# Kernel tuning notes

Measured on AMD Instinct MI355X. Metric: run time of the kernel, lower is better.

The kernel has to match this reference:

```python
import jax, jax.numpy as jnp
import numpy as np

# Pitch / YIN hyperparameters (match init_kwargs)
SR = 8000
HOP = int(round(0.01 * SR))        # 80 samples per hop (hop_time=0.01)
F0_MIN = 60
F0_MAX = 400
THRESH = 0.2
TAU_MIN = SR // F0_MAX             # 20  (smallest lag / highest pitch)
TAU_MAX = SR // F0_MIN             # 133 (largest lag / lowest pitch)
W = TAU_MAX                        # YIN integration window
FRAME_LEN = 2 * TAU_MAX            # need W + TAU_MAX samples per frame


def _yin_f0(x):
    """Batched YIN pitch estimator. x: [B, n_samples] -> f0: [B, n_frames-1].

    Vectorizes the original per-sample Python loop over the whole batch and
    all frames in one pass (difference fn -> CMNDF -> thresholded lag pick).
    """
    B, n = x.shape
    n_frames = 1 + (n - FRAME_LEN) // HOP

    # Frame the signal: [B, F, FRAME_LEN]
    starts = jnp.arange(n_frames) * HOP
    idx = starts[:, None] + jnp.arange(FRAME_LEN)[None, :]
    frames = x[:, idx]

    # Difference function d(tau) = sum_j (x[j] - x[j+tau])^2, tau in [0, TAU_MAX]
    taus = jnp.arange(TAU_MAX + 1)
    sidx = taus[:, None] + jnp.arange(W)[None, :]          # [T+1, W]
    shifted = frames[:, :, sidx]                           # [B, F, T+1, W]
    base = frames[:, :, None, :W]                          # [B, F, 1,  W]
    d = jnp.sum((base - shifted) ** 2, axis=-1)            # [B, F, T+1]

    # Cumulative-mean-normalized difference function (CMNDF)
    eps = jnp.asarray(1e-8, x.dtype)
    cum = jnp.cumsum(d[..., 1:], axis=-1)
    tnum = jnp.arange(1, TAU_MAX + 1, dtype=x.dtype)
    cmndf = d[..., 1:] * tnum / jnp.maximum(cum, eps)      # tau = 1..TAU_MAX
    cmndf = jnp.concatenate([jnp.ones_like(cmndf[..., :1]), cmndf], axis=-1)

    # First lag below threshold (restricted to valid pitch range); else unvoiced
    tau_idx = jnp.arange(TAU_MAX + 1)
    cand = (cmndf < THRESH) & (tau_idx >= TAU_MIN)         # [B, F, T+1]
    voiced = jnp.any(cand, axis=-1)
    tau = jnp.argmax(cand, axis=-1)                        # first True
    f0 = jnp.where(
        voiced,
        jnp.asarray(SR, x.dtype) / jnp.maximum(tau, 1).astype(x.dtype),
        jnp.zeros((), x.dtype),
    )
    # Original forward drops the last frame per sample: f0[0, :-1]
    return f0[:, :-1]


def setup_inputs() -> dict:
    key = jax.random.key(0)
    x = jax.random.normal(key, (8, 80000), dtype=jnp.float32)
    return {"x": x}


def reference(x):
    return _yin_f0(x)
```

## Files before the change

### kernel.cpp

```cpp
#include <hip/hip_runtime.h>


#define NF_OUT 996
#define NSAMP  80000
#define FPB    6
#define BPB    (NF_OUT / FPB)
#define CHUNKD 672
#define TH     0.2f
#define EPS    1e-8f

template<int CTRL>
__device__ __forceinline__ float dpp_add_f(float x) {
    int t = __builtin_amdgcn_update_dpp(0, __builtin_bit_cast(int, x), CTRL, 0xF, 0xF, false);
    return x + __builtin_bit_cast(float, t);
}
__device__ __forceinline__ float dpp_b15_add_f(float x) {
    int t = __builtin_amdgcn_update_dpp(0, __builtin_bit_cast(int, x), 0x142, 0xA, 0xF, false);
    return x + __builtin_bit_cast(float, t);
}
template<int CTRL>
__device__ __forceinline__ int dpp_min_i(int x) {
    int t = __builtin_amdgcn_update_dpp(0x7FFFFFFF, x, CTRL, 0xF, 0xF, false);
    return (t < x) ? t : x;
}
__device__ __forceinline__ int dpp_b15_min_i(int x) {
    int t = __builtin_amdgcn_update_dpp(0x7FFFFFFF, x, 0x142, 0xA, 0xF, false);
    return (t < x) ? t : x;
}
__device__ __forceinline__ float scan32_add(float v) {
    v = dpp_add_f<0x111>(v);
    v = dpp_add_f<0x112>(v);
    v = dpp_add_f<0x114>(v);
    v = dpp_add_f<0x118>(v);
    v = dpp_b15_add_f(v);
    return v;
}
__device__ __forceinline__ int red32_min(int v) {
    v = dpp_min_i<0x111>(v);
    v = dpp_min_i<0x112>(v);
    v = dpp_min_i<0x114>(v);
    v = dpp_min_i<0x118>(v);
    v = dpp_b15_min_i(v);
    return v;
}

#define MAC4(CURV, NXTV, FRV) do {                                             \
    float w0=CURV.y,w1=CURV.z,w2=CURV.w,w3=NXTV.x,w4=NXTV.y,w5=NXTV.z,w6=NXTV.w; \
    float d_;                                                                  \
    d_=FRV.x-w0; a0=fmaf(d_,d_,a0); d_=FRV.y-w1; a0=fmaf(d_,d_,a0);            \
    d_=FRV.z-w2; a0=fmaf(d_,d_,a0); d_=FRV.w-w3; a0=fmaf(d_,d_,a0);            \
    d_=FRV.x-w1; a1=fmaf(d_,d_,a1); d_=FRV.y-w2; a1=fmaf(d_,d_,a1);            \
    d_=FRV.z-w3; a1=fmaf(d_,d_,a1); d_=FRV.w-w4; a1=fmaf(d_,d_,a1);            \
    d_=FRV.x-w2; a2=fmaf(d_,d_,a2); d_=FRV.y-w3; a2=fmaf(d_,d_,a2);            \
    d_=FRV.z-w4; a2=fmaf(d_,d_,a2); d_=FRV.w-w5; a2=fmaf(d_,d_,a2);            \
    d_=FRV.x-w3; a3=fmaf(d_,d_,a3); d_=FRV.y-w4; a3=fmaf(d_,d_,a3);            \
    d_=FRV.z-w5; a3=fmaf(d_,d_,a3); d_=FRV.w-w6; a3=fmaf(d_,d_,a3);            \
} while (0)

__global__ __launch_bounds__(192) void yin_kernel(const float* __restrict__ x,
                                                  float* __restrict__ out) {
    const int bx = blockIdx.x;
    const int b  = bx / BPB;
    const int fb = bx - b * BPB;
    const float* __restrict__ xrow = x + (size_t)b * NSAMP + (size_t)fb * (FPB * 80);

    __shared__ __align__(16) float sch[CHUNKD];
    const int t = threadIdx.x;
    {
        int t4 = t * 4;
        if (t4 < CHUNKD)
            *(float4*)(sch + t4) = *(const float4*)(xrow + t4);
    }
    __syncthreads();

    const int lane = t & 63;
    const int w    = t >> 6;
    const int h    = lane >> 5;
    const int l2   = lane & 31;
    const float* f  = sch + (2 * w + h) * 80;
    const float* gp = f + 4 * l2;

    float4 cur = *(const float4*)(gp);
    const float4 S0 = cur;
    float4 nxt;
    float a0 = 0.f, a1 = 0.f, a2 = 0.f, a3 = 0.f;

    #pragma unroll 4
    for (int c = 0; c < 32; ++c) {
        nxt = *(const float4*)(gp + 4 * (c + 1));
        float4 fr = *(const float4*)(f + 4 * c);
        MAC4(cur, nxt, fr);
        cur = nxt;
    }
    const float4 C32 = cur;
    {
        nxt = *(const float4*)(gp + 4 * 33);
        float4 fr = *(const float4*)(f + 128);
        MAC4(cur, nxt, fr);
        cur = nxt;
    }
    const float4 C33 = cur;
    const float4 C34 = *(const float4*)(gp + 4 * 34);
    {
        float frx = f[132];
        float d_;
        d_ = frx - C33.y; a0 = fmaf(d_, d_, a0);
        d_ = frx - C33.z; a1 = fmaf(d_, d_, a1);
        d_ = frx - C33.w; a2 = fmaf(d_, d_, a2);
        d_ = frx - C34.x; a3 = fmaf(d_, d_, a3);
    }

    float sm[8] = {C32.y, C32.z, C32.w, C33.x, C33.y, C33.z, C33.w, C34.x};
    float s0a[4] = {S0.x, S0.y, S0.z, S0.w};
    float p[5] = {0.f, 0.f, 0.f, 0.f, 0.f};
    #pragma unroll
    for (int k = 0; k < 5; ++k) {
        #pragma unroll
        for (int q = 0; q < 4; ++q) {
            float d_ = s0a[q] - sm[k + q];
            p[k] = fmaf(d_, d_, p[k]);
        }
    }
    if (l2 < 5) {
        float av = f[128 + l2];
        #pragma unroll
        for (int k = 0; k < 5; ++k) {
            float d_ = av - f[257 + l2 + k];
            p[k] = fmaf(d_, d_, p[k]);
        }
    }
    #pragma unroll
    for (int k = 0; k < 5; ++k) p[k] = scan32_add(p[k]);

    float L = a0 + a1 + a2 + a3;
    float inc = scan32_add(L);
    float excl = inc - L;
    float c0 = excl + a0;
    float c1 = c0 + a1;
    float c2 = c1 + a2;
    float c3 = c2 + a3;

    int best = 0x7FFFFFFF;
    const int tau0 = 4 * l2 + 1;
    if (tau0     >= 20 && a0 * (float)(tau0)     < TH * fmaxf(c0, EPS)) best = tau0;
    if (best == 0x7FFFFFFF && tau0 + 1 >= 20 && a1 * (float)(tau0 + 1) < TH * fmaxf(c1, EPS)) best = tau0 + 1;
    if (best == 0x7FFFFFFF && tau0 + 2 >= 20 && a2 * (float)(tau0 + 2) < TH * fmaxf(c2, EPS)) best = tau0 + 2;
    if (best == 0x7FFFFFFF && tau0 + 3 >= 20 && a3 * (float)(tau0 + 3) < TH * fmaxf(c3, EPS)) best = tau0 + 3;

    if (l2 == 31) {
        float cum = c3;
        #pragma unroll
        for (int k = 0; k < 5; ++k) {
            cum += p[k];
            if (p[k] * (float)(129 + k) < TH * fmaxf(cum, EPS))
                best = (best < 129 + k) ? best : (129 + k);
        }
    }
    best = red32_min(best);

    if (l2 == 31) {
        int fr_idx = fb * FPB + 2 * w + h;
        out[(size_t)b * NF_OUT + fr_idx] =
            (best == 0x7FFFFFFF) ? 0.0f : 8000.0f / (float)best;
    }
}

extern "C" void kernel_launch(void* const* d_in, const int* in_sizes, int n_in,
                              void* d_out, int out_size, void* d_ws, size_t ws_size,
                              hipStream_t stream) {
    (void)in_sizes; (void)n_in; (void)d_ws; (void)ws_size; (void)out_size;
    const float* x = (const float*)d_in[0];
    float* out = (float*)d_out;
    yin_kernel<<<dim3(8 * BPB), dim3(192), 0, stream>>>(x, out);
}
```

Baseline: 15.65 us.

## Expand squared difference into energy terms minus cross-correlation

Rewrites the YIN difference function as sum(x^2) + sum(y^2) - 2*sum(x*y). The inner loop now does only one FMA per product instead of a subtract plus an FMA, and the window energies are built separately from a running square sum and a wave scan. It also adds an occupancy hint to the launch bounds. The cancellation in the expanded form can lose float precision near the threshold, which could flip the pick of the first lag below threshold.

```diff
diff --git a/kernel.cpp b/kernel.cpp
--- a/kernel.cpp
+++ b/kernel.cpp
@@ -44,21 +44,22 @@
     return v;
 }
 
-#define MAC4(CURV, NXTV, FRV) do {                                             \
+#define MACR(CURV, NXTV, FRV) do {                                             \
     float w0=CURV.y,w1=CURV.z,w2=CURV.w,w3=NXTV.x,w4=NXTV.y,w5=NXTV.z,w6=NXTV.w; \
-    float d_;                                                                  \
-    d_=FRV.x-w0; a0=fmaf(d_,d_,a0); d_=FRV.y-w1; a0=fmaf(d_,d_,a0);            \
-    d_=FRV.z-w2; a0=fmaf(d_,d_,a0); d_=FRV.w-w3; a0=fmaf(d_,d_,a0);            \
-    d_=FRV.x-w1; a1=fmaf(d_,d_,a1); d_=FRV.y-w2; a1=fmaf(d_,d_,a1);            \
-    d_=FRV.z-w3; a1=fmaf(d_,d_,a1); d_=FRV.w-w4; a1=fmaf(d_,d_,a1);            \
-    d_=FRV.x-w2; a2=fmaf(d_,d_,a2); d_=FRV.y-w3; a2=fmaf(d_,d_,a2);            \
-    d_=FRV.z-w4; a2=fmaf(d_,d_,a2); d_=FRV.w-w5; a2=fmaf(d_,d_,a2);            \
-    d_=FRV.x-w3; a3=fmaf(d_,d_,a3); d_=FRV.y-w4; a3=fmaf(d_,d_,a3);            \
-    d_=FRV.z-w5; a3=fmaf(d_,d_,a3); d_=FRV.w-w6; a3=fmaf(d_,d_,a3);            \
+    r0 = fmaf(FRV.x,w0,r0); r1 = fmaf(FRV.x,w1,r1);                            \
+    r2 = fmaf(FRV.x,w2,r2); r3 = fmaf(FRV.x,w3,r3);                            \
+    r0 = fmaf(FRV.y,w1,r0); r1 = fmaf(FRV.y,w2,r1);                            \
+    r2 = fmaf(FRV.y,w3,r2); r3 = fmaf(FRV.y,w4,r3);                            \
+    r0 = fmaf(FRV.z,w2,r0); r1 = fmaf(FRV.z,w3,r1);                            \
+    r2 = fmaf(FRV.z,w4,r2); r3 = fmaf(FRV.z,w5,r3);                            \
+    r0 = fmaf(FRV.w,w3,r0); r1 = fmaf(FRV.w,w4,r1);                            \
+    r2 = fmaf(FRV.w,w5,r2); r3 = fmaf(FRV.w,w6,r3);                            \
+    Q  = fmaf(NXTV.x,NXTV.x,Q); Q = fmaf(NXTV.y,NXTV.y,Q);                     \
+    Q  = fmaf(NXTV.z,NXTV.z,Q); Q = fmaf(NXTV.w,NXTV.w,Q);                     \
 } while (0)
 
-__global__ __launch_bounds__(192) void yin_kernel(const float* __restrict__ x,
-                                                  float* __restrict__ out) {
+__global__ __launch_bounds__(192, 4) void yin_kernel(const float* __restrict__ x,
+                                                     float* __restrict__ out) {
     const int bx = blockIdx.x;
     const int b  = bx / BPB;
     const int fb = bx - b * BPB;
@@ -83,32 +84,49 @@
     float4 cur = *(const float4*)(gp);
     const float4 S0 = cur;
     float4 nxt;
-    float a0 = 0.f, a1 = 0.f, a2 = 0.f, a3 = 0.f;
+    float r0 = 0.f, r1 = 0.f, r2 = 0.f, r3 = 0.f, Q = 0.f;
 
     #pragma unroll 4
     for (int c = 0; c < 32; ++c) {
         nxt = *(const float4*)(gp + 4 * (c + 1));
         float4 fr = *(const float4*)(f + 4 * c);
-        MAC4(cur, nxt, fr);
+        MACR(cur, nxt, fr);
         cur = nxt;
     }
     const float4 C32 = cur;
+    float4 FR32;
     {
         nxt = *(const float4*)(gp + 4 * 33);
-        float4 fr = *(const float4*)(f + 128);
-        MAC4(cur, nxt, fr);
+        FR32 = *(const float4*)(f + 128);
+        MACR(cur, nxt, FR32);
         cur = nxt;
     }
     const float4 C33 = cur;
     const float4 C34 = *(const float4*)(gp + 4 * 34);
+    const float frx = f[132];
     {
-        float frx = f[132];
-        float d_;
-        d_ = frx - C33.y; a0 = fmaf(d_, d_, a0);
-        d_ = frx - C33.z; a1 = fmaf(d_, d_, a1);
-        d_ = frx - C33.w; a2 = fmaf(d_, d_, a2);
-        d_ = frx - C34.x; a3 = fmaf(d_, d_, a3);
+        r0 = fmaf(frx, C33.y, r0);
+        r1 = fmaf(frx, C33.z, r1);
+        r2 = fmaf(frx, C33.w, r2);
+        r3 = fmaf(frx, C34.x, r3);
     }
+
+    const float sy = S0.y * S0.y, sz = S0.z * S0.z, sw = S0.w * S0.w;
+    const float zC = C33.z * C33.z, wC = C33.w * C33.w, x34 = C34.x * C34.x;
+    const float EB0 = Q + sy + sz + sw - zC - wC;
+    const float EB1 = Q + sz + sw - wC;
+    const float EB2 = Q + sw;
+    const float EB3 = Q + x34;
+
+    float sq4 = fmaf(S0.x, S0.x, fmaf(S0.y, S0.y, fmaf(S0.z, S0.z, S0.w * S0.w)));
+    float tot128 = __shfl(scan32_add(sq4), 31, 32);
+    float EA = tot128 + FR32.x * FR32.x + FR32.y * FR32.y
+             + FR32.z * FR32.z + FR32.w * FR32.w + frx * frx;
+
+    const float a0 = fmaf(-2.f, r0, EA + EB0);
+    const float a1 = fmaf(-2.f, r1, EA + EB1);
+    const float a2 = fmaf(-2.f, r2, EA + EB2);
+    const float a3 = fmaf(-2.f, r3, EA + EB3);
 
     float sm[8] = {C32.y, C32.z, C32.w, C33.x, C33.y, C33.z, C33.w, C34.x};
     float s0a[4] = {S0.x, S0.y, S0.z, S0.w};
```

After: 15.14 us, median of 2. -3.3%, faster.

## Split each frame's lag window across a full wavefront with cross-half reduction

Applied to the files above, without the earlier changes.

Each frame is now processed by one 64-lane wavefront instead of a 32-lane half. The two halves each take half of the integration window and are combined with xor-32 shuffles. The tail lags 129-133 are computed across all 64 lanes with a 64-wide DPP scan. Blocks now hold 4 frames and 256 threads with a launch-bounds occupancy hint, which halves the per-lane MAC loop and raises thread-level parallelism, at the cost of more shuffles and more blocks.

```diff
diff --git a/kernel.cpp b/kernel.cpp
--- a/kernel.cpp
+++ b/kernel.cpp
@@ -3,44 +3,45 @@
 
 #define NF_OUT 996
 #define NSAMP  80000
-#define FPB    6
+#define FPB    4
 #define BPB    (NF_OUT / FPB)
-#define CHUNKD 672
+#define CHUNKD 512
 #define TH     0.2f
 #define EPS    1e-8f
 
-template<int CTRL>
-__device__ __forceinline__ float dpp_add_f(float x) {
-    int t = __builtin_amdgcn_update_dpp(0, __builtin_bit_cast(int, x), CTRL, 0xF, 0xF, false);
+template<int CTRL, int RMASK>
+__device__ __forceinline__ float dpp_add(float x) {
+    int t = __builtin_amdgcn_update_dpp(0, __builtin_bit_cast(int, x), CTRL, RMASK, 0xF, false);
     return x + __builtin_bit_cast(float, t);
 }
-__device__ __forceinline__ float dpp_b15_add_f(float x) {
-    int t = __builtin_amdgcn_update_dpp(0, __builtin_bit_cast(int, x), 0x142, 0xA, 0xF, false);
-    return x + __builtin_bit_cast(float, t);
-}
-template<int CTRL>
-__device__ __forceinline__ int dpp_min_i(int x) {
-    int t = __builtin_amdgcn_update_dpp(0x7FFFFFFF, x, CTRL, 0xF, 0xF, false);
-    return (t < x) ? t : x;
-}
-__device__ __forceinline__ int dpp_b15_min_i(int x) {
-    int t = __builtin_amdgcn_update_dpp(0x7FFFFFFF, x, 0x142, 0xA, 0xF, false);
+template<int CTRL, int RMASK>
+__device__ __forceinline__ int dpp_min(int x) {
+    int t = __builtin_amdgcn_update_dpp(0x7FFFFFFF, x, CTRL, RMASK, 0xF, false);
     return (t < x) ? t : x;
 }
 __device__ __forceinline__ float scan32_add(float v) {
-    v = dpp_add_f<0x111>(v);
-    v = dpp_add_f<0x112>(v);
-    v = dpp_add_f<0x114>(v);
-    v = dpp_add_f<0x118>(v);
-    v = dpp_b15_add_f(v);
+    v = dpp_add<0x111, 0xF>(v);
+    v = dpp_add<0x112, 0xF>(v);
+    v = dpp_add<0x114, 0xF>(v);
+    v = dpp_add<0x118, 0xF>(v);
+    v = dpp_add<0x142, 0xA>(v);
+    return v;
+}
+__device__ __forceinline__ float scan64_add(float v) {
+    v = dpp_add<0x111, 0xF>(v);
+    v = dpp_add<0x112, 0xF>(v);
+    v = dpp_add<0x114, 0xF>(v);
+    v = dpp_add<0x118, 0xF>(v);
+    v = dpp_add<0x142, 0xA>(v);
+    v = dpp_add<0x143, 0xC>(v);
     return v;
 }
 __device__ __forceinline__ int red32_min(int v) {
-    v = dpp_min_i<0x111>(v);
-    v = dpp_min_i<0x112>(v);
-    v = dpp_min_i<0x114>(v);
-    v = dpp_min_i<0x118>(v);
-    v = dpp_b15_min_i(v);
+    v = dpp_min<0x111, 0xF>(v);
+    v = dpp_min<0x112, 0xF>(v);
+    v = dpp_min<0x114, 0xF>(v);
+    v = dpp_min<0x118, 0xF>(v);
+    v = dpp_min<0x142, 0xA>(v);
     return v;
 }
 
@@ -57,8 +58,8 @@
     d_=FRV.z-w5; a3=fmaf(d_,d_,a3); d_=FRV.w-w6; a3=fmaf(d_,d_,a3);            \
 } while (0)
 
-__global__ __launch_bounds__(192) void yin_kernel(const float* __restrict__ x,
-                                                  float* __restrict__ out) {
+__global__ __launch_bounds__(256, 6) void yin_kernel(const float* __restrict__ x,
+                                                     float* __restrict__ out) {
     const int bx = blockIdx.x;
     const int b  = bx / BPB;
     const int fb = bx - b * BPB;
@@ -66,71 +67,66 @@
 
     __shared__ __align__(16) float sch[CHUNKD];
     const int t = threadIdx.x;
-    {
-        int t4 = t * 4;
-        if (t4 < CHUNKD)
-            *(float4*)(sch + t4) = *(const float4*)(xrow + t4);
-    }
+    if (t < 128)
+        *(float4*)(sch + 4 * t) = *(const float4*)(xrow + 4 * t);
     __syncthreads();
 
     const int lane = t & 63;
     const int w    = t >> 6;
     const int h    = lane >> 5;
     const int l2   = lane & 31;
-    const float* f  = sch + (2 * w + h) * 80;
-    const float* gp = f + 4 * l2;
+    const float* f   = sch + w * 80;
+    const float* bcp = f + 68 * h;
+    const float* qF  = bcp + 4 * l2;
 
-    float4 cur = *(const float4*)(gp);
-    const float4 S0 = cur;
-    float4 nxt;
+    float4 cur = *(const float4*)(qF);
     float a0 = 0.f, a1 = 0.f, a2 = 0.f, a3 = 0.f;
 
-    #pragma unroll 4
-    for (int c = 0; c < 32; ++c) {
-        nxt = *(const float4*)(gp + 4 * (c + 1));
-        float4 fr = *(const float4*)(f + 4 * c);
+    #pragma unroll 2
+    for (int c = 0; c < 16; ++c) {
+        float4 nxt = *(const float4*)(qF + 4 * c + 4);
+        float4 fr  = *(const float4*)(bcp + 4 * c);
         MAC4(cur, nxt, fr);
         cur = nxt;
     }
-    const float4 C32 = cur;
     {
-        nxt = *(const float4*)(gp + 4 * 33);
-        float4 fr = *(const float4*)(f + 128);
-        MAC4(cur, nxt, fr);
-        cur = nxt;
-    }
-    const float4 C33 = cur;
-    const float4 C34 = *(const float4*)(gp + 4 * 34);
-    {
-        float frx = f[132];
-        float d_;
-        d_ = frx - C33.y; a0 = fmaf(d_, d_, a0);
-        d_ = frx - C33.z; a1 = fmaf(d_, d_, a1);
-        d_ = frx - C33.w; a2 = fmaf(d_, d_, a2);
-        d_ = frx - C34.x; a3 = fmaf(d_, d_, a3);
+        float4 nxt = *(const float4*)(qF + 68);
+        float4 fr  = *(const float4*)(bcp + 64);
+        if (h == 0) {
+            MAC4(cur, nxt, fr);
+        } else {
+            float d_;
+            d_ = fr.x - cur.y; a0 = fmaf(d_, d_, a0);
+            d_ = fr.x - cur.z; a1 = fmaf(d_, d_, a1);
+            d_ = fr.x - cur.w; a2 = fmaf(d_, d_, a2);
+            d_ = fr.x - nxt.x; a3 = fmaf(d_, d_, a3);
+        }
     }
 
-    float sm[8] = {C32.y, C32.z, C32.w, C33.x, C33.y, C33.z, C33.w, C34.x};
-    float s0a[4] = {S0.x, S0.y, S0.z, S0.w};
+    a0 += __shfl_xor(a0, 32);
+    a1 += __shfl_xor(a1, 32);
+    a2 += __shfl_xor(a2, 32);
+    a3 += __shfl_xor(a3, 32);
+
     float p[5] = {0.f, 0.f, 0.f, 0.f, 0.f};
-    #pragma unroll
-    for (int k = 0; k < 5; ++k) {
-        #pragma unroll
-        for (int q = 0; q < 4; ++q) {
-            float d_ = s0a[q] - sm[k + q];
-            p[k] = fmaf(d_, d_, p[k]);
-        }
-    }
-    if (l2 < 5) {
-        float av = f[128 + l2];
+    {
+        float fj1 = f[lane];
+        float fj2 = f[lane + 64];
         #pragma unroll
         for (int k = 0; k < 5; ++k) {
-            float d_ = av - f[257 + l2 + k];
-            p[k] = fmaf(d_, d_, p[k]);
+            float d1 = fj1 - f[lane + 129 + k]; p[k] = fmaf(d1, d1, p[k]);
+            float d2 = fj2 - f[lane + 193 + k]; p[k] = fmaf(d2, d2, p[k]);
+        }
+        if (lane < 5) {
+            float fj3 = f[128 + lane];
+            #pragma unroll
+            for (int k = 0; k < 5; ++k) {
+                float d3 = fj3 - f[257 + lane + k]; p[k] = fmaf(d3, d3, p[k]);
+            }
         }
     }
     #pragma unroll
-    for (int k = 0; k < 5; ++k) p[k] = scan32_add(p[k]);
+    for (int k = 0; k < 5; ++k) p[k] = scan64_add(p[k]);
 
     float L = a0 + a1 + a2 + a3;
     float inc = scan32_add(L);
@@ -147,7 +143,7 @@
     if (best == 0x7FFFFFFF && tau0 + 2 >= 20 && a2 * (float)(tau0 + 2) < TH * fmaxf(c2, EPS)) best = tau0 + 2;
     if (best == 0x7FFFFFFF && tau0 + 3 >= 20 && a3 * (float)(tau0 + 3) < TH * fmaxf(c3, EPS)) best = tau0 + 3;
 
-    if (l2 == 31) {
+    if (lane == 63) {
         float cum = c3;
         #pragma unroll
         for (int k = 0; k < 5; ++k) {
@@ -158,8 +154,8 @@
     }
     best = red32_min(best);
 
-    if (l2 == 31) {
-        int fr_idx = fb * FPB + 2 * w + h;
+    if (lane == 63) {
+        int fr_idx = fb * FPB + w;
         out[(size_t)b * NF_OUT + fr_idx] =
             (best == 0x7FFFFFFF) ? 0.0f : 8000.0f / (float)best;
     }
@@ -171,5 +167,5 @@
     (void)in_sizes; (void)n_in; (void)d_ws; (void)ws_size; (void)out_size;
     const float* x = (const float*)d_in[0];
     float* out = (float*)d_out;
-    yin_kernel<<<dim3(8 * BPB), dim3(192), 0, stream>>>(x, out);
+    yin_kernel<<<dim3(8 * BPB), dim3(256), 0, stream>>>(x, out);
 }
```

Result: slower. 17.21 us (+10.0%).
